# Kernel tuning notes

Measured on AMD Instinct MI355X. Metric: run time of the kernel, lower is better.

Reference implementation:

```python
import jax, jax.numpy as jnp
import numpy as np

EPS = 1e-5

def _ln(x, w, b, axes):
    mu = jnp.mean(x, axis=axes, keepdims=True)
    var = jnp.mean((x - mu) ** 2, axis=axes, keepdims=True)
    return (x - mu) / jnp.sqrt(var + EPS) * w + b

def setup_inputs() -> dict:
    key = jax.random.key(0)
    ks = jax.random.split(key, 6)
    B, L, D, A, H, F = 1, 1024, 512, 32, 8, 2048
    s = 0.02
    return {
        "x": jax.random.normal(ks[0], (B, L, D), jnp.float32),
        "ln0_w": jnp.ones((D,), jnp.float32),
        "ln0_b": jnp.zeros((D,), jnp.float32),
        "ln1_w": jnp.ones((D, H), jnp.float32),
        "ln1_b": jnp.zeros((D, H), jnp.float32),
        "qw": jax.random.normal(ks[1], (D, A * H), jnp.float32) * s,
        "qb": jnp.zeros((A * H,), jnp.float32),
        "kw": jax.random.normal(ks[2], (D, A * H), jnp.float32) * s,
        "kb": jnp.zeros((A * H,), jnp.float32),
        "vw": jax.random.normal(ks[3], (D, D * H), jnp.float32) * s,
        "vb": jnp.zeros((D * H,), jnp.float32),
        "w1": jax.random.normal(ks[4], (D * H, F), jnp.float32) * s,
        "b1": jnp.zeros((F,), jnp.float32),
        "w2": jax.random.normal(ks[5], (F, D), jnp.float32) * s,
        "b2": jnp.zeros((D,), jnp.float32),
    }

def reference(x, ln0_w, ln0_b, ln1_w, ln1_b, qw, qb, kw, kb, vw, vb, w1, b1, w2, b2):
    B, L, D = x.shape
    H = ln1_w.shape[-1]
    _x = _ln(x, ln0_w, ln0_b, -1)
    # q, k: [B, L, d_att, H] with exp(clamp(.)) feature map
    q = jnp.exp(jnp.clip(_x @ qw + qb, -10.0, 10.0)).reshape(B, L, -1, H)
    k = jnp.exp(jnp.clip(_x @ kw + kb, -10.0, 10.0)).reshape(B, L, -1, H)
    # v uses raw x (not layernormed): [B, L, D, H]
    v = (x @ vw + vb).reshape(B, L, D, H)
    # cumulative outer-product KV state: [B, L, d_att, D, H]
    kv = jnp.cumsum(jnp.einsum('blah,bldh->bladh', k, v), axis=1)
    qkv = jnp.einsum('blah,bladh->bldh', q, kv)          # [B, L, D, H]
    den = jnp.einsum('blah,blah->blh', q, jnp.cumsum(k, axis=1))[..., None, :]  # [B, L, 1, H]
    y = x[..., None] + _ln(qkv / den, ln1_w, ln1_b, (-2, -1))  # LN over (D, H) jointly
    y = y.reshape(B, L, D * H)
    h1 = jax.nn.relu(y @ w1 + b1)
    return jax.nn.relu(h1 @ w2 + b2) + x
```

## Files before the change

kernel.cpp:

```cpp
#include <hip/hip_runtime.h>
#include <hip/hip_bf16.h>
#include <math.h>

#define L_SEQ 1024
#define D_DIM 512
#define A_DIM 32
#define H_DIM 8
#define F_DIM 2048
#define AH 256
#define DH 4096
#define NC 16
#define CH 64
#define QKN 512
#define EPS_LN 1e-5f

typedef __attribute__((ext_vector_type(8))) short short8;
typedef __attribute__((ext_vector_type(4))) float floatx4;

#define ASYNC_COPY16(gp, lp)                                                     \
    __builtin_amdgcn_global_load_lds(                                            \
        (const __attribute__((address_space(1))) void*)(const void*)(gp),        \
        (__attribute__((address_space(3))) void*)(void*)(lp), 16, 0, 0)

__global__ __launch_bounds__(256) void prep_kernel(const float* __restrict__ x,
                                                   const float* __restrict__ ln0w,
                                                   const float* __restrict__ ln0b,
                                                   const float* __restrict__ qw,
                                                   const float* __restrict__ kw,
                                                   const float* __restrict__ vw,
                                                   const float* __restrict__ w1,
                                                   const float* __restrict__ w2,
                                                   __hip_bfloat16* __restrict__ xn,
                                                   __hip_bfloat16* __restrict__ xb,
                                                   __hip_bfloat16* __restrict__ qkwt,
                                                   __hip_bfloat16* __restrict__ vwt,
                                                   __hip_bfloat16* __restrict__ w1t,
                                                   __hip_bfloat16* __restrict__ w2t) {
    __shared__ float tt[32][33];
    __shared__ float red[8];
    int bid = blockIdx.x;
    int tid = threadIdx.x;
    if (bid < 1024) {
        int l = bid;
        float v0 = x[l * D_DIM + tid];
        float v1 = x[l * D_DIM + 256 + tid];
        float s = v0 + v1, s2 = v0 * v0 + v1 * v1;
        for (int off = 32; off > 0; off >>= 1) {
            s += __shfl_down(s, off);
            s2 += __shfl_down(s2, off);
        }
        int lane = tid & 63, wid = tid >> 6;
        if (lane == 0) { red[wid] = s; red[4 + wid] = s2; }
        __syncthreads();
        float ts = red[0] + red[1] + red[2] + red[3];
        float t2 = red[4] + red[5] + red[6] + red[7];
        float mu = ts / (float)D_DIM;
        float var = t2 / (float)D_DIM - mu * mu;
        float rs = rsqrtf(var + EPS_LN);
        xn[l * D_DIM + tid]       = (__hip_bfloat16)((v0 - mu) * rs * ln0w[tid] + ln0b[tid]);
        xn[l * D_DIM + 256 + tid] = (__hip_bfloat16)((v1 - mu) * rs * ln0w[256 + tid] + ln0b[256 + tid]);
        xb[l * D_DIM + tid]       = (__hip_bfloat16)v0;
        xb[l * D_DIM + 256 + tid] = (__hip_bfloat16)v1;
        return;
    }
    const float* in;
    __hip_bfloat16* out;
    int R, C, mode = 0, t;
    if (bid < 1152)      { t = bid - 1024;  in = qw; out = qkwt;                      R = 512;  C = 256; }
    else if (bid < 1280) { t = bid - 1152;  in = kw; out = qkwt + (size_t)AH * D_DIM; R = 512;  C = 256; }
    else if (bid < 3328) { t = bid - 1280;  in = vw; out = vwt;  mode = 1;            R = 512;  C = 4096; }
    else if (bid < 11520){ t = bid - 3328;  in = w1; out = w1t;                       R = 4096; C = 2048; }
    else                 { t = bid - 11520; in = w2; out = w2t;                       R = 2048; C = 512; }
    int ctiles = C >> 5;
    int cx = t % ctiles, cy = t / ctiles;
    int tx = tid & 31, ti = tid >> 5;
    int r0 = cy * 32, c0 = cx * 32;
#pragma unroll
    for (int ii = 0; ii < 4; ++ii)
        tt[ti + ii * 8][tx] = in[(size_t)(r0 + ti + ii * 8) * C + c0 + tx];
    __syncthreads();
#pragma unroll
    for (int ii = 0; ii < 4; ++ii) {
        int c = c0 + ti + ii * 8;
        int orow = mode ? (((c & 7) << 9) | (c >> 3)) : c;
        out[(size_t)orow * R + r0 + tx] = (__hip_bfloat16)tt[tx][ti + ii * 8];
    }
}

__device__ __forceinline__ void gemm_core(const __hip_bfloat16* __restrict__ A,
                                          const __hip_bfloat16* __restrict__ Bt,
                                          int K, int bm, int bn, int k_beg, int k_end,
                                          __hip_bfloat16* As, __hip_bfloat16* Bs,
                                          floatx4 acc[2][2]) {
    const int tid = threadIdx.x;
    const int w = tid >> 6, lane = tid & 63;
    const int wm = (w >> 1) * 32, wn = (w & 1) * 32;
    const int quad = lane >> 4, l16 = lane & 15;
    const int srow = tid >> 4, sslot = tid & 15;
    const int scg = sslot ^ srow;
    for (int k0 = k_beg; k0 < k_end; k0 += 128) {
        __syncthreads();
#pragma unroll
        for (int j = 0; j < 4; ++j) {
            ASYNC_COPY16(A + (size_t)(bm + j * 16 + srow) * K + k0 + scg * 8,
                         As + j * 2048 + w * 512);
            ASYNC_COPY16(Bt + (size_t)(bn + j * 16 + srow) * K + k0 + scg * 8,
                         Bs + j * 2048 + w * 512);
        }
        __syncthreads();
#pragma unroll
        for (int ks = 0; ks < 4; ++ks) {
            short8 af[2], bfr[2];
#pragma unroll
            for (int mt = 0; mt < 2; ++mt) {
                int rr = wm + mt * 16 + l16;
                af[mt] = *(const short8*)(As + rr * 128 + (((ks * 4 + quad) ^ (rr & 15)) * 8));
            }
#pragma unroll
            for (int nt = 0; nt < 2; ++nt) {
                int rr = wn + nt * 16 + l16;
                bfr[nt] = *(const short8*)(Bs + rr * 128 + (((ks * 4 + quad) ^ (rr & 15)) * 8));
            }
#pragma unroll
            for (int mt = 0; mt < 2; ++mt)
#pragma unroll
                for (int nt = 0; nt < 2; ++nt)
                    acc[mt][nt] = __builtin_amdgcn_mfma_f32_16x16x32_bf16(
                        af[mt], bfr[nt], acc[mt][nt], 0, 0, 0);
        }
    }
}

__global__ __launch_bounds__(256) void qkv_gemm(const __hip_bfloat16* __restrict__ xn,
                                                const __hip_bfloat16* __restrict__ xb,
                                                const __hip_bfloat16* __restrict__ qkwt,
                                                const __hip_bfloat16* __restrict__ vwt,
                                                const float* __restrict__ qb,
                                                const float* __restrict__ kb,
                                                const float* __restrict__ vb,
                                                float* __restrict__ qk,
                                                __hip_bfloat16* __restrict__ v) {
    __shared__ __align__(16) __hip_bfloat16 As[64 * 128];
    __shared__ __align__(16) __hip_bfloat16 Bs[64 * 128];
    const int tid = threadIdx.x;
    const int w = tid >> 6, lane = tid & 63;
    const int wm = (w >> 1) * 32, wn = (w & 1) * 32;
    const int quad = lane >> 4, l16 = lane & 15;
    int bid = blockIdx.x;
    bool isv = bid < 1024;
    const __hip_bfloat16 *A, *Bt;
    int bx, by;
    if (isv) {
        int r = bid >> 3;
        bx = (bid & 7) * 8 + (r & 7);
        by = r >> 3;
        A = xb; Bt = vwt;
    } else {
        int b2 = bid - 1024;
        bx = b2 & 7; by = b2 >> 3;
        A = xn; Bt = qkwt;
    }
    const int bm = by * 64, bn = bx * 64;
    floatx4 acc[2][2];
#pragma unroll
    for (int i = 0; i < 2; ++i)
#pragma unroll
        for (int j = 0; j < 2; ++j) acc[i][j] = (floatx4)0.f;
    gemm_core(A, Bt, D_DIM, bm, bn, 0, D_DIM, As, Bs, acc);
#pragma unroll
    for (int mt = 0; mt < 2; ++mt)
#pragma unroll
        for (int nt = 0; nt < 2; ++nt)
#pragma unroll
            for (int r = 0; r < 4; ++r) {
                int row = bm + wm + mt * 16 + quad * 4 + r;
                int col = bn + wn + nt * 16 + l16;
                float val = acc[mt][nt][r];
                if (isv) {
                    int bi = ((col & 511) << 3) | (col >> 9);
                    v[(size_t)row * DH + col] = (__hip_bfloat16)(val + vb[bi]);
                } else {
                    float bb = (col < 256) ? qb[col] : kb[col - 256];
                    qk[(size_t)row * QKN + col] = expf(fminf(fmaxf(val + bb, -10.f), 10.f));
                }
            }
}

template <int STRIP>
__global__ __launch_bounds__(256) void gemm_split(const __hip_bfloat16* __restrict__ A,
                                                  const __hip_bfloat16* __restrict__ Bt,
                                                  float* __restrict__ part,
                                                  int M, int N, int K, int Ksub) {
    __shared__ __align__(16) __hip_bfloat16 As[64 * 128];
    __shared__ __align__(16) __hip_bfloat16 Bs[64 * 128];
    const int tid = threadIdx.x;
    const int w = tid >> 6, lane = tid & 63;
    const int wm = (w >> 1) * 32, wn = (w & 1) * 32;
    const int quad = lane >> 4, l16 = lane & 15;
    int bid = blockIdx.x;
    int r = bid >> 3;
    int bx = (bid & 7) * STRIP + (r % STRIP);
    int by = r / STRIP;
    const int bm = by * 64, bn = bx * 64;
    const int kz = blockIdx.z;
    floatx4 acc[2][2];
#pragma unroll
    for (int i = 0; i < 2; ++i)
#pragma unroll
        for (int j = 0; j < 2; ++j) acc[i][j] = (floatx4)0.f;
    gemm_core(A, Bt, K, bm, bn, kz * Ksub, kz * Ksub + Ksub, As, Bs, acc);
#pragma unroll
    for (int mt = 0; mt < 2; ++mt)
#pragma unroll
        for (int nt = 0; nt < 2; ++nt)
#pragma unroll
            for (int rr = 0; rr < 4; ++rr) {
                int row = bm + wm + mt * 16 + quad * 4 + rr;
                int col = bn + wn + nt * 16 + l16;
                part[((size_t)kz * M + row) * N + col] = acc[mt][nt][rr];
            }
}

__global__ __launch_bounds__(256) void w1red(const float* __restrict__ part,
                                             const float* __restrict__ b1,
                                             __hip_bfloat16* __restrict__ h1) {
    size_t e = ((size_t)blockIdx.x * 256 + threadIdx.x) * 4;
    const size_t MN = (size_t)L_SEQ * F_DIM;
    float4 p0 = *(const float4*)(part + e);
    float4 p1 = *(const float4*)(part + MN + e);
    float4 bb = *(const float4*)(b1 + (e & (F_DIM - 1)));
    h1[e + 0] = (__hip_bfloat16)fmaxf(p0.x + p1.x + bb.x, 0.f);
    h1[e + 1] = (__hip_bfloat16)fmaxf(p0.y + p1.y + bb.y, 0.f);
    h1[e + 2] = (__hip_bfloat16)fmaxf(p0.z + p1.z + bb.z, 0.f);
    h1[e + 3] = (__hip_bfloat16)fmaxf(p0.w + p1.w + bb.w, 0.f);
}

__global__ __launch_bounds__(256) void w2red(const float* __restrict__ part,
                                             const float* __restrict__ b2,
                                             const float* __restrict__ x,
                                             float* __restrict__ out) {
    size_t e = ((size_t)blockIdx.x * 256 + threadIdx.x) * 4;
    const size_t MN = (size_t)L_SEQ * D_DIM;
    float4 v0 = *(const float4*)(part + e);
    float4 v1 = *(const float4*)(part + MN + e);
    float4 v2 = *(const float4*)(part + 2 * MN + e);
    float4 v3 = *(const float4*)(part + 3 * MN + e);
    float4 bb = *(const float4*)(b2 + (e & 511));
    float4 xx = *(const float4*)(x + e);
    float4 r;
    r.x = fmaxf(v0.x + v1.x + v2.x + v3.x + bb.x, 0.f) + xx.x;
    r.y = fmaxf(v0.y + v1.y + v2.y + v3.y + bb.y, 0.f) + xx.y;
    r.z = fmaxf(v0.z + v1.z + v2.z + v3.z + bb.z, 0.f) + xx.z;
    r.w = fmaxf(v0.w + v1.w + v2.w + v3.w + bb.w, 0.f) + xx.w;
    *(float4*)(out + e) = r;
}

__global__ __launch_bounds__(256) void kvchunk_kernel(const float* __restrict__ qk,
                                                      const __hip_bfloat16* __restrict__ v,
                                                      float* __restrict__ S,
                                                      float* __restrict__ Ka) {
    int c = blockIdx.x, h = blockIdx.y, dq = blockIdx.z;
    int tid = threadIdx.x;
    __shared__ __align__(16) __hip_bfloat16 kaT[32][72];
    __shared__ __align__(16) __hip_bfloat16 Vl[128][72];
    for (int e = tid; e < 2048; e += 256) {
        int l = e >> 5, a = e & 31;
        kaT[a][l] = (__hip_bfloat16)qk[(c * CH + l) * QKN + 256 + a * 8 + h];
    }
#pragma unroll
    for (int it = 0; it < 4; ++it) {
        int r = tid + it * 256;
        int l = r >> 4, dg8 = (r & 15) * 8;
        short8 vv = *(const short8*)(v + (size_t)(c * CH + l) * DH + h * D_DIM + dq * 128 + dg8);
#pragma unroll
        for (int j = 0; j < 8; ++j)
            Vl[dg8 + j][l] = ((const __hip_bfloat16*)&vv)[j];
    }
    __syncthreads();
    int w = tid >> 6, lane = tid & 63, quad = lane >> 4, l16 = lane & 15;
    floatx4 acc[2][2];
#pragma unroll
    for (int i = 0; i < 2; ++i)
#pragma unroll
        for (int j = 0; j < 2; ++j) acc[i][j] = (floatx4)0.f;
#pragma unroll
    for (int ks = 0; ks < 2; ++ks) {
        short8 af[2], bfr[2];
#pragma unroll
        for (int mt = 0; mt < 2; ++mt)
            af[mt] = *(const short8*)&kaT[mt * 16 + l16][ks * 32 + quad * 8];
#pragma unroll
        for (int nt = 0; nt < 2; ++nt)
            bfr[nt] = *(const short8*)&Vl[w * 32 + nt * 16 + l16][ks * 32 + quad * 8];
#pragma unroll
        for (int mt = 0; mt < 2; ++mt)
#pragma unroll
            for (int nt = 0; nt < 2; ++nt)
                acc[mt][nt] = __builtin_amdgcn_mfma_f32_16x16x32_bf16(
                    af[mt], bfr[nt], acc[mt][nt], 0, 0, 0);
    }
#pragma unroll
    for (int mt = 0; mt < 2; ++mt)
#pragma unroll
        for (int nt = 0; nt < 2; ++nt)
#pragma unroll
            for (int r = 0; r < 4; ++r) {
                int a = mt * 16 + quad * 4 + r;
                int d = dq * 128 + w * 32 + nt * 16 + l16;
                S[(size_t)((c * A_DIM + a) * H_DIM + h) * D_DIM + d] = acc[mt][nt][r];
            }
    if (dq == 0 && tid < 32) {
        float s = 0.f;
        for (int l = 0; l < CH; ++l) s += (float)kaT[tid][l];
        Ka[c * AH + tid * 8 + h] = s;
    }
}

__global__ __launch_bounds__(256) void scan_kernel(const float* __restrict__ S,
                                                   const float* __restrict__ Ka,
                                                   __hip_bfloat16* __restrict__ P2,
                                                   float* __restrict__ KaP) {
    int dt = blockIdx.x, h = blockIdx.y;
    int tid = threadIdx.x;
    __shared__ float t[32][33];
    int dloc = tid & 31, arow = tid >> 5;
    float run[4] = {0.f, 0.f, 0.f, 0.f};
    int dw = tid >> 3, a4 = (tid & 7) * 4;
    for (int c = 0; c < NC; ++c) {
#pragma unroll
        for (int i = 0; i < 4; ++i) t[arow + 8 * i][dloc] = run[i];
        __syncthreads();
        __hip_bfloat16 o[4];
#pragma unroll
        for (int j = 0; j < 4; ++j) o[j] = (__hip_bfloat16)t[a4 + j][dw];
        *(float2*)&P2[((size_t)((c * 8 + h) * 512 + dt * 32 + dw)) * 32 + a4] = *(float2*)o;
#pragma unroll
        for (int i = 0; i < 4; ++i)
            run[i] += S[(size_t)((c * A_DIM + arow + 8 * i) * H_DIM + h) * D_DIM + dt * 32 + dloc];
        __syncthreads();
    }
    if (dt == 0 && tid < 32) {
        float rk = 0.f;
        for (int c = 0; c < NC; ++c) {
            KaP[c * AH + tid * 8 + h] = rk;
            rk += Ka[c * AH + tid * 8 + h];
        }
    }
}

__global__ __launch_bounds__(256) void passC_kernel(const float* __restrict__ qk,
                                                    const __hip_bfloat16* __restrict__ v,
                                                    const __hip_bfloat16* __restrict__ P2,
                                                    const float* __restrict__ KaP,
                                                    __hip_bfloat16* __restrict__ qkv,
                                                    float* __restrict__ den) {
    int c = blockIdx.x, h = blockIdx.y, dq = blockIdx.z;
    int tid = threadIdx.x;
    __shared__ __align__(16) __hip_bfloat16 qa[64][40];
    __shared__ __align__(16) __hip_bfloat16 ka[64][40];
    __shared__ __align__(16) __hip_bfloat16 Vl[128][72];
    __shared__ __align__(16) __hip_bfloat16 Sc[64][72];
    __shared__ float KaPs[32];
    for (int e = tid; e < 2048; e += 256) {
        int l = e >> 5, a = e & 31;
        int gi = (c * CH + l) * QKN + a * 8 + h;
        qa[l][a] = (__hip_bfloat16)qk[gi];
        ka[l][a] = (__hip_bfloat16)qk[gi + 256];
    }
#pragma unroll
    for (int it = 0; it < 4; ++it) {
        int r = tid + it * 256;
        int l = r >> 4, dg8 = (r & 15) * 8;
        short8 vv = *(const short8*)(v + (size_t)(c * CH + l) * DH + h * D_DIM + dq * 128 + dg8);
#pragma unroll
        for (int j = 0; j < 8; ++j)
            Vl[dg8 + j][l] = ((const __hip_bfloat16*)&vv)[j];
    }
    if (dq == 0 && tid < 32) KaPs[tid] = KaP[c * AH + tid * 8 + h];
    __syncthreads();
    int w = tid >> 6, lane = tid & 63, quad = lane >> 4, l16 = lane & 15;
    short8 afq = *(const short8*)&qa[w * 16 + l16][quad * 8];
    floatx4 sacc[4];
#pragma unroll
    for (int nt = 0; nt < 4; ++nt) sacc[nt] = (floatx4)0.f;
#pragma unroll
    for (int nt = 0; nt < 4; ++nt) {
        short8 bfr = *(const short8*)&ka[nt * 16 + l16][quad * 8];
        sacc[nt] = __builtin_amdgcn_mfma_f32_16x16x32_bf16(afq, bfr, sacc[nt], 0, 0, 0);
    }
#pragma unroll
    for (int nt = 0; nt < 4; ++nt)
#pragma unroll
        for (int r = 0; r < 4; ++r) {
            int l = w * 16 + quad * 4 + r;
            int lp = nt * 16 + l16;
            Sc[l][lp] = (__hip_bfloat16)((lp <= l) ? sacc[nt][r] : 0.f);
        }
    __syncthreads();
    if (dq == 0 && tid < 64) {
        int l = tid;
        float s = 0.f;
        for (int lp = 0; lp <= l; ++lp) s += (float)Sc[l][lp];
        for (int a = 0; a < A_DIM; ++a) s += (float)qa[l][a] * KaPs[a];
        den[(c * CH + l) * H_DIM + h] = s;
    }
    floatx4 acc[8];
#pragma unroll
    for (int nt = 0; nt < 8; ++nt) acc[nt] = (floatx4)0.f;
#pragma unroll
    for (int nt = 0; nt < 8; ++nt) {
        short8 pb = *(const short8*)(P2 + ((size_t)((c * 8 + h) * 512 + dq * 128 + nt * 16 + l16)) * 32 + quad * 8);
        acc[nt] = __builtin_amdgcn_mfma_f32_16x16x32_bf16(afq, pb, acc[nt], 0, 0, 0);
    }
#pragma unroll
    for (int ks = 0; ks < 2; ++ks) {
        short8 afs = *(const short8*)&Sc[w * 16 + l16][ks * 32 + quad * 8];
#pragma unroll
        for (int nt = 0; nt < 8; ++nt) {
            short8 bfr = *(const short8*)&Vl[nt * 16 + l16][ks * 32 + quad * 8];
            acc[nt] = __builtin_amdgcn_mfma_f32_16x16x32_bf16(afs, bfr, acc[nt], 0, 0, 0);
        }
    }
#pragma unroll
    for (int nt = 0; nt < 8; ++nt)
#pragma unroll
        for (int r = 0; r < 4; ++r) {
            int l = w * 16 + quad * 4 + r;
            int d = dq * 128 + nt * 16 + l16;
            qkv[(size_t)(c * CH + l) * DH + h * D_DIM + d] = (__hip_bfloat16)acc[nt][r];
        }
}

__global__ __launch_bounds__(256) void ln1_kernel(const __hip_bfloat16* __restrict__ qkv,
                                                  const float* __restrict__ den,
                                                  const float* __restrict__ x,
                                                  const float* __restrict__ w,
                                                  const float* __restrict__ b,
                                                  __hip_bfloat16* __restrict__ y) {
    int l = blockIdx.x, tid = threadIdx.x;
    __shared__ float dsh[8];
    __shared__ float yl[DH];
    __shared__ float red[8];
    if (tid < 8) dsh[tid] = den[l * H_DIM + tid];
    __syncthreads();
    float t[16];
    float s = 0.f, s2 = 0.f;
#pragma unroll
    for (int j = 0; j < 16; ++j) {
        int e = j * 256 + tid;
        float val = (float)qkv[(size_t)l * DH + e] / dsh[e >> 9];
        t[j] = val;
        s += val;
        s2 += val * val;
    }
    for (int off = 32; off > 0; off >>= 1) {
        s += __shfl_down(s, off);
        s2 += __shfl_down(s2, off);
    }
    int lane = tid & 63, wid = tid >> 6;
    if (lane == 0) { red[wid] = s; red[4 + wid] = s2; }
    __syncthreads();
    float ts = red[0] + red[1] + red[2] + red[3];
    float t2 = red[4] + red[5] + red[6] + red[7];
    float mu = ts / (float)DH;
    float var = t2 / (float)DH - mu * mu;
    float rs = rsqrtf(var + EPS_LN);
#pragma unroll
    for (int j = 0; j < 16; ++j) {
        int e = j * 256 + tid;
        int h = e >> 9, d = e & 511;
        int dh = d * H_DIM + h;
        yl[dh] = x[l * D_DIM + d] + (t[j] - mu) * rs * w[dh] + b[dh];
    }
    __syncthreads();
#pragma unroll
    for (int j = 0; j < 16; ++j) {
        int e = j * 256 + tid;
        y[(size_t)l * DH + e] = (__hip_bfloat16)yl[e];
    }
}

extern "C" void kernel_launch(void* const* d_in, const int* in_sizes, int n_in,
                              void* d_out, int out_size, void* d_ws, size_t ws_size,
                              hipStream_t stream) {
    const float* x     = (const float*)d_in[0];
    const float* ln0_w = (const float*)d_in[1];
    const float* ln0_b = (const float*)d_in[2];
    const float* ln1_w = (const float*)d_in[3];
    const float* ln1_b = (const float*)d_in[4];
    const float* qw    = (const float*)d_in[5];
    const float* qb    = (const float*)d_in[6];
    const float* kw    = (const float*)d_in[7];
    const float* kb    = (const float*)d_in[8];
    const float* vw    = (const float*)d_in[9];
    const float* vb    = (const float*)d_in[10];
    const float* w1    = (const float*)d_in[11];
    const float* b1    = (const float*)d_in[12];
    const float* w2    = (const float*)d_in[13];
    const float* b2    = (const float*)d_in[14];
    float* out = (float*)d_out;

    char* ws = (char*)d_ws;
    __hip_bfloat16* xn_bf = (__hip_bfloat16*)(ws + 0);
    __hip_bfloat16* xbf   = (__hip_bfloat16*)(ws + 1048576);
    __hip_bfloat16* qkwt  = (__hip_bfloat16*)(ws + 2097152);
    __hip_bfloat16* vwt   = (__hip_bfloat16*)(ws + 2621440);
    __hip_bfloat16* w1t   = (__hip_bfloat16*)(ws + 6815744);
    __hip_bfloat16* w2t   = (__hip_bfloat16*)(ws + 23592960);
    float* qk  = (float*)(ws + 25690112);
    __hip_bfloat16* vb16 = (__hip_bfloat16*)(ws + 27787264);
    float* S   = (float*)(ws + 36175872);
    __hip_bfloat16* P2 = (__hip_bfloat16*)(ws + 44564480);
    __hip_bfloat16* qkvb = (__hip_bfloat16*)(ws + 52953088);
    float* Ka  = (float*)(ws + 61341696);
    float* den = (float*)(ws + 61358080);
    float* KaP = (float*)(ws + 61390848);
    float* w1part = (float*)(ws + 61440000);
    __hip_bfloat16* y  = (__hip_bfloat16*)(ws + 44564480);
    __hip_bfloat16* h1 = (__hip_bfloat16*)S;
    float* w2part = (float*)qkvb;

    prep_kernel<<<12544, 256, 0, stream>>>(x, ln0_w, ln0_b, qw, kw, vw, w1, w2,
                                           xn_bf, xbf, qkwt, vwt, w1t, w2t);
    qkv_gemm<<<1152, 256, 0, stream>>>(xn_bf, xbf, qkwt, vwt, qb, kb, vb, qk, vb16);
    kvchunk_kernel<<<dim3(NC, H_DIM, 4), 256, 0, stream>>>(qk, vb16, S, Ka);
    scan_kernel<<<dim3(16, 8), 256, 0, stream>>>(S, Ka, P2, KaP);
    passC_kernel<<<dim3(NC, H_DIM, 4), 256, 0, stream>>>(qk, vb16, P2, KaP, qkvb, den);
    ln1_kernel<<<L_SEQ, 256, 0, stream>>>(qkvb, den, x, ln1_w, ln1_b, y);
    gemm_split<4><<<dim3(512, 1, 2), 256, 0, stream>>>(y, w1t, w1part,
                                                       L_SEQ, F_DIM, DH, DH / 2);
    w1red<<<(L_SEQ * F_DIM) / 1024, 256, 0, stream>>>(w1part, b1, h1);
    gemm_split<1><<<dim3(128, 1, 4), 256, 0, stream>>>(h1, w2t, w2part,
                                                       L_SEQ, D_DIM, F_DIM, F_DIM / 4);
    w2red<<<(L_SEQ * D_DIM) / 1024, 256, 0, stream>>>(w2part, b2, x, out);

    (void)in_sizes; (void)n_in; (void)out_size; (void)ws_size;
}
```

Before: 229.8 us.

## Store V transposed and re-layout S so chunk kernels read MFMA operands directly

The QKV GEMM now writes V in a transposed [D*H, L] bf16 layout through an LDS transpose, which lets the chunk kernels load MFMA B fragments straight from global memory instead of transposing V into LDS. The chunk-state S is also staged through LDS and written in a [c][h][d][a] layout with vectorized stores. This lets the scan become a flat, fully coalesced float4 prefix sum over 128 blocks, with no shared-memory transposes. In exchange, passC reads V from global memory repeatedly with 16-byte loads rather than from LDS.

```diff
diff --git a/kernel.cpp b/kernel.cpp
--- a/kernel.cpp
+++ b/kernel.cpp
@@ -15,6 +15,7 @@
 #define EPS_LN 1e-5f
 
 typedef __attribute__((ext_vector_type(8))) short short8;
+typedef __attribute__((ext_vector_type(4))) short short4v;
 typedef __attribute__((ext_vector_type(4))) float floatx4;
 
 #define ASYNC_COPY16(gp, lp)                                                     \
@@ -139,7 +140,7 @@
                                                 const float* __restrict__ kb,
                                                 const float* __restrict__ vb,
                                                 float* __restrict__ qk,
-                                                __hip_bfloat16* __restrict__ v) {
+                                                __hip_bfloat16* __restrict__ vT) {
     __shared__ __align__(16) __hip_bfloat16 As[64 * 128];
     __shared__ __align__(16) __hip_bfloat16 Bs[64 * 128];
     const int tid = threadIdx.x;
@@ -167,23 +168,43 @@
 #pragma unroll
         for (int j = 0; j < 2; ++j) acc[i][j] = (floatx4)0.f;
     gemm_core(A, Bt, D_DIM, bm, bn, 0, D_DIM, As, Bs, acc);
-#pragma unroll
-    for (int mt = 0; mt < 2; ++mt)
-#pragma unroll
-        for (int nt = 0; nt < 2; ++nt)
-#pragma unroll
-            for (int r = 0; r < 4; ++r) {
-                int row = bm + wm + mt * 16 + quad * 4 + r;
+    if (isv) {
+        __syncthreads();
+        __hip_bfloat16* Ct = As;
+#pragma unroll
+        for (int mt = 0; mt < 2; ++mt)
+#pragma unroll
+            for (int nt = 0; nt < 2; ++nt) {
                 int col = bn + wn + nt * 16 + l16;
-                float val = acc[mt][nt][r];
-                if (isv) {
-                    int bi = ((col & 511) << 3) | (col >> 9);
-                    v[(size_t)row * DH + col] = (__hip_bfloat16)(val + vb[bi]);
-                } else {
+                int bi = ((col & 511) << 3) | (col >> 9);
+                float bbv = vb[bi];
+                __hip_bfloat16 tmp[4];
+#pragma unroll
+                for (int r = 0; r < 4; ++r)
+                    tmp[r] = (__hip_bfloat16)(acc[mt][nt][r] + bbv);
+                *(short4v*)&Ct[(wn + nt * 16 + l16) * 72 + wm + mt * 16 + quad * 4] =
+                    *(short4v*)tmp;
+            }
+        __syncthreads();
+        int colloc = tid >> 2, seg = (tid & 3) * 16;
+        short8 o0 = *(const short8*)&Ct[colloc * 72 + seg];
+        short8 o1 = *(const short8*)&Ct[colloc * 72 + seg + 8];
+        *(short8*)(vT + (size_t)(bn + colloc) * 1024 + bm + seg) = o0;
+        *(short8*)(vT + (size_t)(bn + colloc) * 1024 + bm + seg + 8) = o1;
+    } else {
+#pragma unroll
+        for (int mt = 0; mt < 2; ++mt)
+#pragma unroll
+            for (int nt = 0; nt < 2; ++nt)
+#pragma unroll
+                for (int r = 0; r < 4; ++r) {
+                    int row = bm + wm + mt * 16 + quad * 4 + r;
+                    int col = bn + wn + nt * 16 + l16;
                     float bb = (col < 256) ? qb[col] : kb[col - 256];
-                    qk[(size_t)row * QKN + col] = expf(fminf(fmaxf(val + bb, -10.f), 10.f));
+                    qk[(size_t)row * QKN + col] =
+                        expf(fminf(fmaxf(acc[mt][nt][r] + bb, -10.f), 10.f));
                 }
-            }
+    }
 }
 
 template <int STRIP>
@@ -256,26 +277,17 @@
 }
 
 __global__ __launch_bounds__(256) void kvchunk_kernel(const float* __restrict__ qk,
-                                                      const __hip_bfloat16* __restrict__ v,
+                                                      const __hip_bfloat16* __restrict__ vT,
                                                       float* __restrict__ S,
                                                       float* __restrict__ Ka) {
     int c = blockIdx.x, h = blockIdx.y, dq = blockIdx.z;
     int tid = threadIdx.x;
     __shared__ __align__(16) __hip_bfloat16 kaT[32][72];
-    __shared__ __align__(16) __hip_bfloat16 Vl[128][72];
+    __shared__ __align__(16) float St[128][36];
     for (int e = tid; e < 2048; e += 256) {
         int l = e >> 5, a = e & 31;
         kaT[a][l] = (__hip_bfloat16)qk[(c * CH + l) * QKN + 256 + a * 8 + h];
     }
-#pragma unroll
-    for (int it = 0; it < 4; ++it) {
-        int r = tid + it * 256;
-        int l = r >> 4, dg8 = (r & 15) * 8;
-        short8 vv = *(const short8*)(v + (size_t)(c * CH + l) * DH + h * D_DIM + dq * 128 + dg8);
-#pragma unroll
-        for (int j = 0; j < 8; ++j)
-            Vl[dg8 + j][l] = ((const __hip_bfloat16*)&vv)[j];
-    }
     __syncthreads();
     int w = tid >> 6, lane = tid & 63, quad = lane >> 4, l16 = lane & 15;
     floatx4 acc[2][2];
@@ -291,7 +303,8 @@
             af[mt] = *(const short8*)&kaT[mt * 16 + l16][ks * 32 + quad * 8];
 #pragma unroll
         for (int nt = 0; nt < 2; ++nt)
-            bfr[nt] = *(const short8*)&Vl[w * 32 + nt * 16 + l16][ks * 32 + quad * 8];
+            bfr[nt] = *(const short8*)(vT + (size_t)(h * 512 + dq * 128 + w * 32 + nt * 16 + l16) * 1024
+                                       + c * 64 + ks * 32 + quad * 8);
 #pragma unroll
         for (int mt = 0; mt < 2; ++mt)
 #pragma unroll
@@ -303,12 +316,14 @@
     for (int mt = 0; mt < 2; ++mt)
 #pragma unroll
         for (int nt = 0; nt < 2; ++nt)
-#pragma unroll
-            for (int r = 0; r < 4; ++r) {
-                int a = mt * 16 + quad * 4 + r;
-                int d = dq * 128 + w * 32 + nt * 16 + l16;
-                S[(size_t)((c * A_DIM + a) * H_DIM + h) * D_DIM + d] = acc[mt][nt][r];
-            }
+            *(floatx4*)&St[w * 32 + nt * 16 + l16][mt * 16 + quad * 4] = acc[mt][nt];
+    __syncthreads();
+    int d = tid >> 1, aseg = (tid & 1) * 16;
+    float* dst = S + (size_t)((c * 8 + h) * 512 + dq * 128 + d) * 32 + aseg;
+    const float* src = &St[d][aseg];
+#pragma unroll
+    for (int j = 0; j < 4; ++j)
+        *(float4*)(dst + j * 4) = *(const float4*)(src + j * 4);
     if (dq == 0 && tid < 32) {
         float s = 0.f;
         for (int l = 0; l < CH; ++l) s += (float)kaT[tid][l];
@@ -320,36 +335,28 @@
                                                    const float* __restrict__ Ka,
                                                    __hip_bfloat16* __restrict__ P2,
                                                    float* __restrict__ KaP) {
-    int dt = blockIdx.x, h = blockIdx.y;
-    int tid = threadIdx.x;
-    __shared__ float t[32][33];
-    int dloc = tid & 31, arow = tid >> 5;
-    float run[4] = {0.f, 0.f, 0.f, 0.f};
-    int dw = tid >> 3, a4 = (tid & 7) * 4;
+    size_t j = ((size_t)blockIdx.x * 256 + threadIdx.x) * 4;
+    const size_t CS = 8 * 512 * 32;
+    float4 run = {0.f, 0.f, 0.f, 0.f};
     for (int c = 0; c < NC; ++c) {
-#pragma unroll
-        for (int i = 0; i < 4; ++i) t[arow + 8 * i][dloc] = run[i];
-        __syncthreads();
-        __hip_bfloat16 o[4];
-#pragma unroll
-        for (int j = 0; j < 4; ++j) o[j] = (__hip_bfloat16)t[a4 + j][dw];
-        *(float2*)&P2[((size_t)((c * 8 + h) * 512 + dt * 32 + dw)) * 32 + a4] = *(float2*)o;
-#pragma unroll
-        for (int i = 0; i < 4; ++i)
-            run[i] += S[(size_t)((c * A_DIM + arow + 8 * i) * H_DIM + h) * D_DIM + dt * 32 + dloc];
-        __syncthreads();
-    }
-    if (dt == 0 && tid < 32) {
+        __hip_bfloat16 o[4] = {(__hip_bfloat16)run.x, (__hip_bfloat16)run.y,
+                               (__hip_bfloat16)run.z, (__hip_bfloat16)run.w};
+        *(short4v*)&P2[c * CS + j] = *(short4v*)o;
+        float4 sv = *(const float4*)(S + c * CS + j);
+        run.x += sv.x; run.y += sv.y; run.z += sv.z; run.w += sv.w;
+    }
+    if (blockIdx.x == 0) {
+        int t = threadIdx.x;
         float rk = 0.f;
         for (int c = 0; c < NC; ++c) {
-            KaP[c * AH + tid * 8 + h] = rk;
-            rk += Ka[c * AH + tid * 8 + h];
+            KaP[c * AH + t] = rk;
+            rk += Ka[c * AH + t];
         }
     }
 }
 
 __global__ __launch_bounds__(256) void passC_kernel(const float* __restrict__ qk,
-                                                    const __hip_bfloat16* __restrict__ v,
+                                                    const __hip_bfloat16* __restrict__ vT,
                                                     const __hip_bfloat16* __restrict__ P2,
                                                     const float* __restrict__ KaP,
                                                     __hip_bfloat16* __restrict__ qkv,
@@ -358,7 +365,6 @@
     int tid = threadIdx.x;
     __shared__ __align__(16) __hip_bfloat16 qa[64][40];
     __shared__ __align__(16) __hip_bfloat16 ka[64][40];
-    __shared__ __align__(16) __hip_bfloat16 Vl[128][72];
     __shared__ __align__(16) __hip_bfloat16 Sc[64][72];
     __shared__ float KaPs[32];
     for (int e = tid; e < 2048; e += 256) {
@@ -367,15 +373,6 @@
         qa[l][a] = (__hip_bfloat16)qk[gi];
         ka[l][a] = (__hip_bfloat16)qk[gi + 256];
     }
-#pragma unroll
-    for (int it = 0; it < 4; ++it) {
-        int r = tid + it * 256;
-        int l = r >> 4, dg8 = (r & 15) * 8;
-        short8 vv = *(const short8*)(v + (size_t)(c * CH + l) * DH + h * D_DIM + dq * 128 + dg8);
-#pragma unroll
-        for (int j = 0; j < 8; ++j)
-            Vl[dg8 + j][l] = ((const __hip_bfloat16*)&vv)[j];
-    }
     if (dq == 0 && tid < 32) KaPs[tid] = KaP[c * AH + tid * 8 + h];
     __syncthreads();
     int w = tid >> 6, lane = tid & 63, quad = lane >> 4, l16 = lane & 15;
@@ -417,7 +414,8 @@
         short8 afs = *(const short8*)&Sc[w * 16 + l16][ks * 32 + quad * 8];
 #pragma unroll
         for (int nt = 0; nt < 8; ++nt) {
-            short8 bfr = *(const short8*)&Vl[nt * 16 + l16][ks * 32 + quad * 8];
+            short8 bfr = *(const short8*)(vT + (size_t)(h * 512 + dq * 128 + nt * 16 + l16) * 1024
+                                          + c * 64 + ks * 32 + quad * 8);
             acc[nt] = __builtin_amdgcn_mfma_f32_16x16x32_bf16(afs, bfr, acc[nt], 0, 0, 0);
         }
     }
@@ -508,7 +506,7 @@
     __hip_bfloat16* w1t   = (__hip_bfloat16*)(ws + 6815744);
     __hip_bfloat16* w2t   = (__hip_bfloat16*)(ws + 23592960);
     float* qk  = (float*)(ws + 25690112);
-    __hip_bfloat16* vb16 = (__hip_bfloat16*)(ws + 27787264);
+    __hip_bfloat16* vT = (__hip_bfloat16*)(ws + 27787264);
     float* S   = (float*)(ws + 36175872);
     __hip_bfloat16* P2 = (__hip_bfloat16*)(ws + 44564480);
     __hip_bfloat16* qkvb = (__hip_bfloat16*)(ws + 52953088);
@@ -522,10 +520,10 @@
 
     prep_kernel<<<12544, 256, 0, stream>>>(x, ln0_w, ln0_b, qw, kw, vw, w1, w2,
                                            xn_bf, xbf, qkwt, vwt, w1t, w2t);
-    qkv_gemm<<<1152, 256, 0, stream>>>(xn_bf, xbf, qkwt, vwt, qb, kb, vb, qk, vb16);
-    kvchunk_kernel<<<dim3(NC, H_DIM, 4), 256, 0, stream>>>(qk, vb16, S, Ka);
-    scan_kernel<<<dim3(16, 8), 256, 0, stream>>>(S, Ka, P2, KaP);
-    passC_kernel<<<dim3(NC, H_DIM, 4), 256, 0, stream>>>(qk, vb16, P2, KaP, qkvb, den);
+    qkv_gemm<<<1152, 256, 0, stream>>>(xn_bf, xbf, qkwt, vwt, qb, kb, vb, qk, vT);
+    kvchunk_kernel<<<dim3(NC, H_DIM, 4), 256, 0, stream>>>(qk, vT, S, Ka);
+    scan_kernel<<<128, 256, 0, stream>>>(S, Ka, P2, KaP);
+    passC_kernel<<<dim3(NC, H_DIM, 4), 256, 0, stream>>>(qk, vT, P2, KaP, qkvb, den);
     ln1_kernel<<<L_SEQ, 256, 0, stream>>>(qkvb, den, x, ln1_w, ln1_b, y);
     gemm_split<4><<<dim3(512, 1, 2), 256, 0, stream>>>(y, w1t, w1part,
                                                        L_SEQ, F_DIM, DH, DH / 2);
```

New measurement: 213.3 us. 1.08x faster.
